# Optimization experiments

Hardware: AMD Instinct MI355X
Metric: run time of the kernel (lower is better)

## Reference

```python
import jax, jax.numpy as jnp
import numpy as np

B, T, D, H = 4, 2048, 1024, 16
HD = D // H


def setup_inputs() -> dict:
    key = jax.random.key(0)
    ks = jax.random.split(key, 10)
    s = 1.0 / np.sqrt(D)
    # xavier_uniform bound for wbias [T,T]: sqrt(6/(T+T))
    wb_bound = float(np.sqrt(6.0 / (T + T)))
    return {
        "x": jax.random.normal(ks[0], (B, T, D), dtype=jnp.float32),
        "Wq": jax.random.normal(ks[1], (D, D), dtype=jnp.float32) * s,
        "bq": jnp.zeros((D,), dtype=jnp.float32),
        "Wk": jax.random.normal(ks[2], (D, D), dtype=jnp.float32) * s,
        "bk": jnp.zeros((D,), dtype=jnp.float32),
        "Wv": jax.random.normal(ks[3], (D, D), dtype=jnp.float32) * s,
        "bv": jnp.zeros((D,), dtype=jnp.float32),
        "Wo": jax.random.normal(ks[4], (D, D), dtype=jnp.float32) * s,
        "bo": jnp.zeros((D,), dtype=jnp.float32),
        "wbias": jax.random.uniform(ks[5], (T, T), dtype=jnp.float32,
                                    minval=-wb_bound, maxval=wb_bound),
    }


def reference(x, Wq, bq, Wk, bk, Wv, bv, Wo, bo, wbias):
    Bc, Tc, Dc = x.shape
    # projections, split heads: [B, H, T, HD]
    def proj(W, b):
        y = x @ W + b
        return y.reshape(Bc, Tc, H, HD).transpose(0, 2, 1, 3)

    Q = proj(Wq, bq)
    K = proj(Wk, bk)
    V = proj(Wv, bv)

    Q_sig = jax.nn.sigmoid(Q)
    eK = jnp.exp(K)                      # [B,H,T,HD]
    ew = jnp.exp(wbias[:Tc, :Tc])        # [T,T]

    num = jnp.einsum('ts,bhsd->bhtd', ew, eK * V)
    den = jnp.einsum('ts,bhsd->bhtd', ew, eK)
    out = Q_sig * (num / den)            # [B,H,T,HD]

    out = out.transpose(0, 2, 1, 3).reshape(Bc, Tc, Dc)
    return out @ Wo + bo
```

## Files before the change

kernel.cpp:

```cpp
#include <hip/hip_runtime.h>
#include <hip/hip_bf16.h>


#define AS1(p) ((const __attribute__((address_space(1))) void*)(p))
#define AS3(p) ((__attribute__((address_space(3))) void*)(p))

typedef _Float16 half8 __attribute__((ext_vector_type(8)));
typedef _Float16 half4v __attribute__((ext_vector_type(4)));
typedef float floatx16 __attribute__((ext_vector_type(16)));
typedef int intx4 __attribute__((ext_vector_type(4)));
typedef int intx8 __attribute__((ext_vector_type(8)));

__device__ __forceinline__ long frag_off(int r, int k) {
  return (long)(((((r >> 5) * 4 + (k >> 4)) * 2 + ((k >> 3) & 1)) * 32 + (r & 31)) * 8 + (k & 7));
}
__device__ __forceinline__ long off8(int r, int k) {
  return (long)((((((r >> 5) * 2 + ((k >> 6) & 1)) * 2 + ((k >> 4) & 1)) * 2 + ((k >> 5) & 1)) * 32 +
                 (r & 31)) * 16 + (k & 15));
}

__global__ __launch_bounds__(256) void prep_all(
    const float* __restrict__ x, const float* __restrict__ wb, const float* __restrict__ Wq,
    const float* __restrict__ Wk, const float* __restrict__ Wv, const float* __restrict__ Wo,
    _Float16* __restrict__ x_h, char* __restrict__ E8, _Float16* __restrict__ WqkvT,
    _Float16* __restrict__ WoT) {
  __shared__ _Float16 lds[64 * 132];
  const int bid = blockIdx.x;
  const int tid = threadIdx.x;

  if (bid < 1024) {
    const int tm = bid >> 4, tk = bid & 15;
    const long tbase = (long)bid * 8192;
#pragma unroll
    for (int p = 0; p < 4; ++p) {
      const int s = p * 256 + tid;
      const int r = ((s >> 8) << 5) + (s & 31);
      const int k = ((s >> 6) & 3) * 16 + ((s >> 5) & 1) * 8;
      const float* sp = x + (long)(tm * 128 + r) * 1024 + tk * 64 + k;
      const float4 v0 = *(const float4*)sp;
      const float4 v1 = *(const float4*)(sp + 4);
      half8 h;
      h[0] = (_Float16)v0.x; h[1] = (_Float16)v0.y; h[2] = (_Float16)v0.z; h[3] = (_Float16)v0.w;
      h[4] = (_Float16)v1.x; h[5] = (_Float16)v1.y; h[6] = (_Float16)v1.z; h[7] = (_Float16)v1.w;
      *(half8*)(x_h + tbase + (long)s * 8) = h;
    }
    return;
  }

  if (bid >= 1536) {
    const int e = bid - 1536;
    const int tt = e >> 4, ts = e & 15;
    char* dst = E8 + (long)e * 16384;
#pragma unroll
    for (int p = 0; p < 16; ++p) {
      const int idx = p * 256 + tid;
      const int r = idx >> 5, k = (idx & 31) * 4;
      const float4 v = *(const float4*)(wb + (long)(tt * 128 + r) * 2048 + ts * 128 + k);
      const float e0 = (__expf(v.x) - 1.0f) * 32.0f, e1 = (__expf(v.y) - 1.0f) * 32.0f;
      const float e2 = (__expf(v.z) - 1.0f) * 32.0f, e3 = (__expf(v.w) - 1.0f) * 32.0f;
      int pk = __builtin_amdgcn_cvt_pk_fp8_f32(e0, e1, 0, false);
      pk = __builtin_amdgcn_cvt_pk_fp8_f32(e2, e3, pk, true);
      *(int*)(dst + off8(r, k)) = pk;
    }
    return;
  }

  const int b2 = bid - 1024;
  const float* src0;
  const float* src1 = nullptr;
  _Float16* dst;
  int tn, tk, cb = 0;
  if (b2 < 128) {
    tn = b2 >> 4; tk = b2 & 15; src0 = Wq; dst = WqkvT;
  } else if (b2 < 384) {
    const int t = b2 - 128;
    tn = 8 + (t >> 4); tk = t & 15; cb = (tn - 8) * 64; src0 = Wk; src1 = Wv; dst = WqkvT;
  } else {
    const int t = b2 - 384;
    tn = t >> 4; tk = t & 15; src0 = Wo; dst = WoT;
  }
  if (!src1) {
#pragma unroll
    for (int p = 0; p < 8; ++p) {
      const int kl = p * 8 + (tid >> 5);
      const int cl = (tid & 31) * 4;
      const float4 v = *(const float4*)(src0 + (long)(tk * 64 + kl) * 1024 + tn * 128 + cl);
      half4v h;
      h[0] = (_Float16)v.x; h[1] = (_Float16)v.y; h[2] = (_Float16)v.z; h[3] = (_Float16)v.w;
      *(half4v*)(lds + kl * 132 + cl) = h;
    }
  } else {
#pragma unroll
    for (int m = 0; m < 2; ++m) {
      const float* s = m ? src1 : src0;
      const int rb = m ? 32 : 0;
#pragma unroll
      for (int p = 0; p < 4; ++p) {
        const int kl = p * 16 + (tid >> 4);
        const int cl = (tid & 15) * 4;
        const int rl = (cl >> 5) * 64 + rb + (cl & 31);
        const float4 v = *(const float4*)(s + (long)(tk * 64 + kl) * 1024 + cb + cl);
        half4v h;
        h[0] = (_Float16)v.x; h[1] = (_Float16)v.y; h[2] = (_Float16)v.z; h[3] = (_Float16)v.w;
        *(half4v*)(lds + kl * 132 + rl) = h;
      }
    }
  }
  __syncthreads();
  const long tbase = (long)(tn * 16 + tk) * 8192;
#pragma unroll
  for (int p = 0; p < 4; ++p) {
    const int s = p * 256 + tid;
    const int r = ((s >> 8) << 5) + (s & 31);
    const int kl = ((s >> 6) & 3) * 16 + ((s >> 5) & 1) * 8;
    half8 h;
#pragma unroll
    for (int j = 0; j < 8; ++j) h[j] = lds[(kl + j) * 132 + r];
    *(half8*)(dst + tbase + (long)s * 8) = h;
  }
}

template <int VM>
__device__ __forceinline__ void aft_phase(int g, const _Float16* __restrict__ Ablk,
                                          const _Float16* __restrict__ Bblk,
                                          _Float16* ring, int tid, int wid, int lane,
                                          int wm, int wn, floatx16 (&acc)[2][2]) {
  const _Float16* slotA = ring + (g & 3) * 4096;
  const _Float16* slotB = ring + 16384 + (g & 3) * 8192;
  half8 af[2][2], bf[2][2];
#pragma unroll
  for (int mt = 0; mt < 2; ++mt)
#pragma unroll
    for (int ks = 0; ks < 2; ++ks)
      af[mt][ks] = *(const half8*)(slotA + ((wm >> 5) + mt) * 1024 + ks * 512 + lane * 8);
#pragma unroll
  for (int nt = 0; nt < 2; ++nt)
#pragma unroll
    for (int ks = 0; ks < 2; ++ks)
      bf[nt][ks] = *(const half8*)(slotB + ((wn >> 5) + nt) * 1024 + ks * 512 + lane * 8);
  const int gs = g + 3;
  if (gs < 32) {
    const int t = gs >> 1;
    const long goff = (long)(tid >> 7) * 2048 + (gs & 1) * 1024 + (tid & 127) * 8;
    _Float16* dA = ring + (gs & 3) * 4096 + wid * 512;
    _Float16* dB = ring + 16384 + (gs & 3) * 8192 + wid * 512;
    __builtin_amdgcn_global_load_lds(AS1(Ablk + (long)t * 8192 + goff), AS3(dA), 16, 0, 0);
    __builtin_amdgcn_global_load_lds(AS1(Bblk + (long)t * 8192 + goff), AS3(dB), 16, 0, 0);
    __builtin_amdgcn_global_load_lds(AS1(Bblk + (long)(16 + t) * 8192 + goff), AS3(dB + 4096),
                                     16, 0, 0);
  }
  asm volatile("s_waitcnt vmcnt(%0)" ::"i"(VM) : "memory");
  __builtin_amdgcn_s_barrier();
  asm volatile("s_waitcnt lgkmcnt(0)" ::: "memory");
  __builtin_amdgcn_s_setprio(1);
#pragma unroll
  for (int ks = 0; ks < 2; ++ks)
#pragma unroll
    for (int mt = 0; mt < 2; ++mt)
#pragma unroll
      for (int nt = 0; nt < 2; ++nt)
        acc[mt][nt] =
            __builtin_amdgcn_mfma_f32_32x32x16_f16(af[mt][ks], bf[nt][ks], acc[mt][nt], 0, 0, 0);
  __builtin_amdgcn_s_setprio(0);
  __builtin_amdgcn_s_barrier();
  asm volatile("" ::: "memory");
}

template <int MODE>
__global__ __launch_bounds__(512, 2) void gemm_bt2(
    const _Float16* __restrict__ A, const _Float16* __restrict__ Bt, void* __restrict__ Cv,
    const float* __restrict__ bias0, const float* __restrict__ bias1,
    const float* __restrict__ bias2, char* __restrict__ Zt8, float* __restrict__ cs) {
  __shared__ __align__(16) _Float16 ring[49152];
  const int tid = threadIdx.x;
  const int wid = tid >> 6, lane = tid & 63;
  const int l32 = lane & 31, khalf = lane >> 5;

  const int f = blockIdx.x;
  const int j = f >> 3;
  const int bxs = (f & 7) * 8 + (j & 7);
  const int bys = j >> 3;
  const int m0 = bxs * 128, n0 = bys * 256;
  const int wm = (wid >> 2) * 64, wn = (wid & 3) * 64;

  const _Float16* Ablk = A + (long)bxs * 131072;
  const _Float16* Bblk = Bt + (long)(bys * 2) * 131072;

#pragma unroll
  for (int g0 = 0; g0 < 3; ++g0) {
    const int t = g0 >> 1;
    const long goff = (long)(tid >> 7) * 2048 + (g0 & 1) * 1024 + (tid & 127) * 8;
    __builtin_amdgcn_global_load_lds(AS1(Ablk + (long)t * 8192 + goff),
                                     AS3(ring + g0 * 4096 + wid * 512), 16, 0, 0);
    __builtin_amdgcn_global_load_lds(AS1(Bblk + (long)t * 8192 + goff),
                                     AS3(ring + 16384 + g0 * 8192 + wid * 512), 16, 0, 0);
    __builtin_amdgcn_global_load_lds(AS1(Bblk + (long)(16 + t) * 8192 + goff),
                                     AS3(ring + 16384 + g0 * 8192 + 4096 + wid * 512), 16, 0, 0);
  }
  asm volatile("s_waitcnt vmcnt(6)" ::: "memory");
  __builtin_amdgcn_s_barrier();
  asm volatile("" ::: "memory");

  floatx16 acc[2][2] = {};
#pragma unroll 1
  for (int gb = 0; gb < 28; gb += 4) {
    aft_phase<6>(gb + 0, Ablk, Bblk, ring, tid, wid, lane, wm, wn, acc);
    aft_phase<6>(gb + 1, Ablk, Bblk, ring, tid, wid, lane, wm, wn, acc);
    aft_phase<6>(gb + 2, Ablk, Bblk, ring, tid, wid, lane, wm, wn, acc);
    aft_phase<6>(gb + 3, Ablk, Bblk, ring, tid, wid, lane, wm, wn, acc);
  }
  aft_phase<6>(28, Ablk, Bblk, ring, tid, wid, lane, wm, wn, acc);
  aft_phase<3>(29, Ablk, Bblk, ring, tid, wid, lane, wm, wn, acc);
  aft_phase<0>(30, Ablk, Bblk, ring, tid, wid, lane, wm, wn, acc);
  aft_phase<0>(31, Ablk, Bblk, ring, tid, wid, lane, wm, wn, acc);

  if (MODE == 0) {
    if (n0 < 1024) {
      _Float16* Qs = (_Float16*)Cv;
#pragma unroll
      for (int mt = 0; mt < 2; ++mt) {
        const long ttile = (m0 + wm + mt * 32) >> 5;
#pragma unroll
        for (int nt = 0; nt < 2; ++nt) {
          const int col = n0 + wn + nt * 32 + l32;
          const float bb = bias0[col];
          const long base = (ttile * 32 + (((n0 + wn) >> 5) + nt)) * 1024;
#pragma unroll
          for (int q = 0; q < 4; ++q) {
            half4v o;
#pragma unroll
            for (int rr = 0; rr < 4; ++rr) {
              const float v = acc[mt][nt][q * 4 + rr] + bb;
              o[rr] = (_Float16)(1.0f / (1.0f + __expf(-v)));
            }
            *(half4v*)(Qs + base + q * 256 + lane * 4) = o;
          }
        }
      }
    } else {
      const int grp = (n0 - 1024 + wn) >> 6;
      const int ch = grp * 32 + l32;
      const float bkc = bias1[ch], bvc = bias2[ch];
      const int jn = grp * 64 + l32;
      const int b = m0 >> 11;
      char* Z8 = Zt8 + (long)b * 4194304 +
                 ((long)(jn >> 7) * 16 + ((m0 & 2047) >> 7)) * 16384;
      const int jnl = jn & 127;
      float sk = 0.f, sz = 0.f;
#pragma unroll
      for (int mt = 0; mt < 2; ++mt) {
#pragma unroll
        for (int q = 0; q < 4; ++q) {
          float ekv[4], ekk[4];
#pragma unroll
          for (int rr = 0; rr < 4; ++rr) {
            const float ek = __expf(acc[mt][0][q * 4 + rr] + bkc);
            const float vv = acc[mt][1][q * 4 + rr] + bvc;
            ekk[rr] = ek;
            ekv[rr] = ek * vv;
            sk += ek;
            sz += ek * vv;
          }
          const int sl = wm + mt * 32 + 4 * khalf + 8 * q;
          int pn = __builtin_amdgcn_cvt_pk_fp8_f32(ekv[0] * 0.25f, ekv[1] * 0.25f, 0, false);
          pn = __builtin_amdgcn_cvt_pk_fp8_f32(ekv[2] * 0.25f, ekv[3] * 0.25f, pn, true);
          int pd = __builtin_amdgcn_cvt_pk_fp8_f32(ekk[0] * 0.25f, ekk[1] * 0.25f, 0, false);
          pd = __builtin_amdgcn_cvt_pk_fp8_f32(ekk[2] * 0.25f, ekk[3] * 0.25f, pd, true);
          *(int*)(Z8 + off8(jnl, sl)) = pn;
          *(int*)(Z8 + off8(jnl + 32, sl)) = pd;
        }
      }
      atomicAdd(&cs[(long)b * 2048 + ch * 2], sz);
      atomicAdd(&cs[(long)b * 2048 + ch * 2 + 1], sk);
    }
    return;
  }

#pragma unroll
  for (int mt = 0; mt < 2; ++mt)
#pragma unroll
    for (int nt = 0; nt < 2; ++nt) {
      const int col = n0 + wn + nt * 32 + l32;
      const float bb = bias0[col];
#pragma unroll
      for (int reg = 0; reg < 16; ++reg) {
        const int row = m0 + wm + mt * 32 + 4 * khalf + 8 * (reg >> 2) + (reg & 3);
        ((float*)Cv)[(long)row * 1024 + col] = acc[mt][nt][reg] + bb;
      }
    }
}

__global__ __launch_bounds__(256) void gemm2_fp8(
    const char* __restrict__ E8, const char* __restrict__ Zt8, _Float16* __restrict__ OH,
    const _Float16* __restrict__ Qsig, const float* __restrict__ cs) {
  __shared__ __align__(16) char sA[16384];
  __shared__ __align__(16) char sB[16384];
  const int tid = threadIdx.x;
  const int wave = tid >> 6, lane = tid & 63;
  const int l32 = lane & 31, khalf = lane >> 5;

  const int f = blockIdx.x + 16 * (blockIdx.y + 16 * blockIdx.z);
  const int nid = (f & 7) * 128 + (f >> 3);
  const int bxs = nid & 15, bys = (nid >> 4) & 15, bzs = nid >> 8;

  const int m0 = bxs * 128, n0 = bys * 128;
  const int wm = (wave >> 1) * 64, wn = (wave & 1) * 64;

  const char* At = E8 + (long)bxs * 16 * 16384;
  const char* Bt = Zt8 + (long)bzs * 4194304 + (long)bys * 16 * 16384;

  floatx16 acc[2][2] = {};

  for (int tk = 0; tk < 16; ++tk) {
    const char* As = At + tk * 16384 + wave * 1024 + lane * 16;
    const char* Bs = Bt + tk * 16384 + wave * 1024 + lane * 16;
#pragma unroll
    for (int c = 0; c < 4; ++c) {
      __builtin_amdgcn_global_load_lds(AS1(As + c * 4096), AS3(sA + c * 4096 + wave * 1024), 16, 0, 0);
      __builtin_amdgcn_global_load_lds(AS1(Bs + c * 4096), AS3(sB + c * 4096 + wave * 1024), 16, 0, 0);
    }
    __syncthreads();
#pragma unroll
    for (int ks = 0; ks < 2; ++ks) {
      intx8 a8[2], b8[2];
#pragma unroll
      for (int i = 0; i < 2; ++i) {
        const char* pa = sA + (((wm >> 5) + i) * 2 + ks) * 2048 + khalf * 512 + l32 * 16;
        const intx4 alo = *(const intx4*)pa;
        const intx4 ahi = *(const intx4*)(pa + 1024);
        a8[i] = __builtin_shufflevector(alo, ahi, 0, 1, 2, 3, 4, 5, 6, 7);
        const char* pb = sB + (((wn >> 5) + i) * 2 + ks) * 2048 + khalf * 512 + l32 * 16;
        const intx4 blo = *(const intx4*)pb;
        const intx4 bhi = *(const intx4*)(pb + 1024);
        b8[i] = __builtin_shufflevector(blo, bhi, 0, 1, 2, 3, 4, 5, 6, 7);
      }
#pragma unroll
      for (int mt = 0; mt < 2; ++mt)
#pragma unroll
        for (int nt = 0; nt < 2; ++nt)
          acc[mt][nt] = __builtin_amdgcn_mfma_scale_f32_32x32x64_f8f6f4(
              a8[mt], b8[nt], acc[mt][nt], 0, 0, 0, 127u, 0, 127u);
    }
    __syncthreads();
  }

  const int ch = ((n0 + wn) >> 6) * 32 + l32;
  const float2 c2 = *(const float2*)(cs + (long)bzs * 2048 + ch * 2);
#pragma unroll
  for (int mt = 0; mt < 2; ++mt) {
    const long ttile = (long)(bzs * 2048 + m0 + wm + mt * 32) >> 5;
    const long qbase = (ttile * 32 + ((n0 + wn) >> 6)) * 1024;
#pragma unroll
    for (int q = 0; q < 4; ++q) {
      const half4v qv = *(const half4v*)(Qsig + qbase + q * 256 + lane * 4);
#pragma unroll
      for (int rr = 0; rr < 4; ++rr) {
        const int reg = q * 4 + rr;
        const float num = c2.x + acc[mt][0][reg] * 0.125f;
        const float den = c2.y + acc[mt][1][reg] * 0.125f;
        const int r = m0 + wm + mt * 32 + 4 * khalf + 8 * q + rr;
        const int R = bzs * 2048 + r;
        const long off = ((long)(R >> 7) * 16 + (ch >> 6)) * 8192 + frag_off(R & 127, ch & 63);
        OH[off] = (_Float16)((float)qv[rr] * num / den);
      }
    }
  }
}

extern "C" void kernel_launch(void* const* d_in, const int* in_sizes, int n_in, void* d_out,
                              int out_size, void* d_ws, size_t ws_size, hipStream_t stream) {
  const float* x = (const float*)d_in[0];
  const float* Wq = (const float*)d_in[1];
  const float* bq = (const float*)d_in[2];
  const float* Wk = (const float*)d_in[3];
  const float* bk = (const float*)d_in[4];
  const float* Wv = (const float*)d_in[5];
  const float* bv = (const float*)d_in[6];
  const float* Wo = (const float*)d_in[7];
  const float* bo = (const float*)d_in[8];
  const float* wb = (const float*)d_in[9];

  char* ws = (char*)d_ws;
  _Float16* x_h = (_Float16*)(ws + 0);
  _Float16* WqkvT = (_Float16*)(ws + 16777216);
  _Float16* WoT = (_Float16*)(ws + 23068672);
  char* E8 = (char*)(ws + 25165824);
  _Float16* Qsig = (_Float16*)(ws + 29360128);
  char* Zt8 = (char*)(ws + 46137344);
  _Float16* OutHead = (_Float16*)(ws + 62914560);
  float* cs = (float*)(ws + 79691776);

  hipMemsetAsync(cs, 0, 4 * 2048 * sizeof(float), stream);

  prep_all<<<1792, 256, 0, stream>>>(x, wb, Wq, Wk, Wv, Wo, x_h, E8, WqkvT, WoT);

  gemm_bt2<0><<<768, 512, 0, stream>>>(x_h, WqkvT, Qsig, bq, bk, bv, Zt8, cs);

  gemm2_fp8<<<dim3(16, 16, 4), 256, 0, stream>>>(E8, Zt8, OutHead, Qsig, cs);

  gemm_bt2<2><<<256, 512, 0, stream>>>(OutHead, WoT, d_out, bo, nullptr, nullptr, nullptr, nullptr);
}
```

Baseline: 250.7 us.

## Use 4-wave GEMM blocks with 64x128 warp tiles and 3-slot LDS ring

The projection GEMMs now run 256-thread blocks in place of 512, so each wave computes a 64x128 output tile (2x4 MFMA accumulators) instead of 64x64. The LDS ring shrinks from four slots to three, and the global-to-LDS prefetch is issued with per-thread precomputed pointers. The vmcnt wait moves after the MFMAs so loads overlap compute. This raises per-wave register reuse and cuts LDS footprint, at the cost of more accumulator registers and fewer waves available to hide latency.

```diff
diff --git a/kernel.cpp b/kernel.cpp
--- a/kernel.cpp
+++ b/kernel.cpp
@@ -120,37 +120,31 @@
   }
 }
 
-template <int VM>
-__device__ __forceinline__ void aft_phase(int g, const _Float16* __restrict__ Ablk,
-                                          const _Float16* __restrict__ Bblk,
-                                          _Float16* ring, int tid, int wid, int lane,
-                                          int wm, int wn, floatx16 (&acc)[2][2]) {
-  const _Float16* slotA = ring + (g & 3) * 4096;
-  const _Float16* slotB = ring + 16384 + (g & 3) * 8192;
-  half8 af[2][2], bf[2][2];
+template <int VM, bool STAGE>
+__device__ __forceinline__ void aft_phase2(
+    const _Float16* rA, const _Float16* rB, _Float16* sAd, _Float16* sBd,
+    const _Float16* gA, const _Float16* gB, int lane, int wm, int wn,
+    floatx16 (&acc)[2][4]) {
+  half8 af[2][2], bf[4][2];
 #pragma unroll
   for (int mt = 0; mt < 2; ++mt)
 #pragma unroll
     for (int ks = 0; ks < 2; ++ks)
-      af[mt][ks] = *(const half8*)(slotA + ((wm >> 5) + mt) * 1024 + ks * 512 + lane * 8);
-#pragma unroll
-  for (int nt = 0; nt < 2; ++nt)
+      af[mt][ks] = *(const half8*)(rA + (((wm >> 5) + mt) * 2 + ks) * 512 + lane * 8);
+#pragma unroll
+  for (int nt = 0; nt < 4; ++nt)
 #pragma unroll
     for (int ks = 0; ks < 2; ++ks)
-      bf[nt][ks] = *(const half8*)(slotB + ((wn >> 5) + nt) * 1024 + ks * 512 + lane * 8);
-  const int gs = g + 3;
-  if (gs < 32) {
-    const int t = gs >> 1;
-    const long goff = (long)(tid >> 7) * 2048 + (gs & 1) * 1024 + (tid & 127) * 8;
-    _Float16* dA = ring + (gs & 3) * 4096 + wid * 512;
-    _Float16* dB = ring + 16384 + (gs & 3) * 8192 + wid * 512;
-    __builtin_amdgcn_global_load_lds(AS1(Ablk + (long)t * 8192 + goff), AS3(dA), 16, 0, 0);
-    __builtin_amdgcn_global_load_lds(AS1(Bblk + (long)t * 8192 + goff), AS3(dB), 16, 0, 0);
-    __builtin_amdgcn_global_load_lds(AS1(Bblk + (long)(16 + t) * 8192 + goff), AS3(dB + 4096),
-                                     16, 0, 0);
-  }
-  asm volatile("s_waitcnt vmcnt(%0)" ::"i"(VM) : "memory");
-  __builtin_amdgcn_s_barrier();
+      bf[nt][ks] = *(const half8*)(rB + (((wn >> 5) + nt) * 2 + ks) * 512 + lane * 8);
+  if (STAGE) {
+#pragma unroll
+    for (int p = 0; p < 2; ++p)
+      __builtin_amdgcn_global_load_lds(AS1(gA + p * 4096), AS3(sAd + p * 2048), 16, 0, 0);
+#pragma unroll
+    for (int q = 0; q < 4; ++q)
+      __builtin_amdgcn_global_load_lds(AS1(gB + (q >> 1) * 131072 + (q & 1) * 4096),
+                                       AS3(sBd + q * 2048), 16, 0, 0);
+  }
   asm volatile("s_waitcnt lgkmcnt(0)" ::: "memory");
   __builtin_amdgcn_s_setprio(1);
 #pragma unroll
@@ -158,20 +152,21 @@
 #pragma unroll
     for (int mt = 0; mt < 2; ++mt)
 #pragma unroll
-      for (int nt = 0; nt < 2; ++nt)
+      for (int nt = 0; nt < 4; ++nt)
         acc[mt][nt] =
             __builtin_amdgcn_mfma_f32_32x32x16_f16(af[mt][ks], bf[nt][ks], acc[mt][nt], 0, 0, 0);
   __builtin_amdgcn_s_setprio(0);
+  asm volatile("s_waitcnt vmcnt(%0)" ::"i"(VM) : "memory");
   __builtin_amdgcn_s_barrier();
   asm volatile("" ::: "memory");
 }
 
 template <int MODE>
-__global__ __launch_bounds__(512, 2) void gemm_bt2(
+__global__ __launch_bounds__(256, 2) void gemm_bt2(
     const _Float16* __restrict__ A, const _Float16* __restrict__ Bt, void* __restrict__ Cv,
     const float* __restrict__ bias0, const float* __restrict__ bias1,
     const float* __restrict__ bias2, char* __restrict__ Zt8, float* __restrict__ cs) {
-  __shared__ __align__(16) _Float16 ring[49152];
+  __shared__ __align__(16) _Float16 ring[36864];
   const int tid = threadIdx.x;
   const int wid = tid >> 6, lane = tid & 63;
   const int l32 = lane & 31, khalf = lane >> 5;
@@ -181,38 +176,48 @@
   const int bxs = (f & 7) * 8 + (j & 7);
   const int bys = j >> 3;
   const int m0 = bxs * 128, n0 = bys * 256;
-  const int wm = (wid >> 2) * 64, wn = (wid & 3) * 64;
-
-  const _Float16* Ablk = A + (long)bxs * 131072;
-  const _Float16* Bblk = Bt + (long)(bys * 2) * 131072;
-
-#pragma unroll
-  for (int g0 = 0; g0 < 3; ++g0) {
-    const int t = g0 >> 1;
-    const long goff = (long)(tid >> 7) * 2048 + (g0 & 1) * 1024 + (tid & 127) * 8;
-    __builtin_amdgcn_global_load_lds(AS1(Ablk + (long)t * 8192 + goff),
-                                     AS3(ring + g0 * 4096 + wid * 512), 16, 0, 0);
-    __builtin_amdgcn_global_load_lds(AS1(Bblk + (long)t * 8192 + goff),
-                                     AS3(ring + 16384 + g0 * 8192 + wid * 512), 16, 0, 0);
-    __builtin_amdgcn_global_load_lds(AS1(Bblk + (long)(16 + t) * 8192 + goff),
-                                     AS3(ring + 16384 + g0 * 8192 + 4096 + wid * 512), 16, 0, 0);
+  const int wm = (wid >> 1) * 64, wn = (wid & 1) * 128;
+
+  const long thrOff = (long)(tid >> 7) * 2048 + (tid & 127) * 8;
+  const _Float16* gA0 = A + (long)bxs * 131072 + thrOff;
+  const _Float16* gB0 = Bt + (long)(bys * 2) * 131072 + thrOff;
+
+  _Float16* ringB = ring + 12288;
+  _Float16* sAt = ring + tid * 8;
+  _Float16* sBt = ringB + tid * 8;
+
+#pragma unroll
+  for (int ph = 0; ph < 2; ++ph) {
+    const _Float16* ga = gA0 + ph * 1024;
+    const _Float16* gb = gB0 + ph * 1024;
+#pragma unroll
+    for (int p = 0; p < 2; ++p)
+      __builtin_amdgcn_global_load_lds(AS1(ga + p * 4096), AS3(sAt + ph * 4096 + p * 2048), 16, 0, 0);
+#pragma unroll
+    for (int q = 0; q < 4; ++q)
+      __builtin_amdgcn_global_load_lds(AS1(gb + (q >> 1) * 131072 + (q & 1) * 4096),
+                                       AS3(sBt + ph * 8192 + q * 2048), 16, 0, 0);
   }
   asm volatile("s_waitcnt vmcnt(6)" ::: "memory");
   __builtin_amdgcn_s_barrier();
   asm volatile("" ::: "memory");
 
-  floatx16 acc[2][2] = {};
-#pragma unroll 1
-  for (int gb = 0; gb < 28; gb += 4) {
-    aft_phase<6>(gb + 0, Ablk, Bblk, ring, tid, wid, lane, wm, wn, acc);
-    aft_phase<6>(gb + 1, Ablk, Bblk, ring, tid, wid, lane, wm, wn, acc);
-    aft_phase<6>(gb + 2, Ablk, Bblk, ring, tid, wid, lane, wm, wn, acc);
-    aft_phase<6>(gb + 3, Ablk, Bblk, ring, tid, wid, lane, wm, wn, acc);
-  }
-  aft_phase<6>(28, Ablk, Bblk, ring, tid, wid, lane, wm, wn, acc);
-  aft_phase<3>(29, Ablk, Bblk, ring, tid, wid, lane, wm, wn, acc);
-  aft_phase<0>(30, Ablk, Bblk, ring, tid, wid, lane, wm, wn, acc);
-  aft_phase<0>(31, Ablk, Bblk, ring, tid, wid, lane, wm, wn, acc);
+  floatx16 acc[2][4] = {};
+
+#pragma unroll
+  for (int pr = 0; pr < 15; ++pr) {
+    const int s0 = (2 * pr) % 3, s1 = (2 * pr + 1) % 3, s2 = (2 * pr + 2) % 3;
+    const _Float16* gA = gA0 + (long)(pr + 1) * 8192;
+    const _Float16* gB = gB0 + (long)(pr + 1) * 8192;
+    aft_phase2<6, true>(ring + s0 * 4096, ringB + s0 * 8192, sAt + s2 * 4096, sBt + s2 * 8192,
+                        gA, gB, lane, wm, wn, acc);
+    aft_phase2<6, true>(ring + s1 * 4096, ringB + s1 * 8192, sAt + s0 * 4096, sBt + s0 * 8192,
+                        gA + 1024, gB + 1024, lane, wm, wn, acc);
+  }
+  aft_phase2<0, false>(ring + 0 * 4096, ringB + 0 * 8192, nullptr, nullptr, nullptr, nullptr,
+                       lane, wm, wn, acc);
+  aft_phase2<0, false>(ring + 1 * 4096, ringB + 1 * 8192, nullptr, nullptr, nullptr, nullptr,
+                       lane, wm, wn, acc);
 
   if (MODE == 0) {
     if (n0 < 1024) {
@@ -221,7 +226,7 @@
       for (int mt = 0; mt < 2; ++mt) {
         const long ttile = (m0 + wm + mt * 32) >> 5;
 #pragma unroll
-        for (int nt = 0; nt < 2; ++nt) {
+        for (int nt = 0; nt < 4; ++nt) {
           const int col = n0 + wn + nt * 32 + l32;
           const float bb = bias0[col];
           const long base = (ttile * 32 + (((n0 + wn) >> 5) + nt)) * 1024;
@@ -238,40 +243,44 @@
         }
       }
     } else {
-      const int grp = (n0 - 1024 + wn) >> 6;
-      const int ch = grp * 32 + l32;
-      const float bkc = bias1[ch], bvc = bias2[ch];
-      const int jn = grp * 64 + l32;
       const int b = m0 >> 11;
-      char* Z8 = Zt8 + (long)b * 4194304 +
-                 ((long)(jn >> 7) * 16 + ((m0 & 2047) >> 7)) * 16384;
-      const int jnl = jn & 127;
-      float sk = 0.f, sz = 0.f;
-#pragma unroll
-      for (int mt = 0; mt < 2; ++mt) {
-#pragma unroll
-        for (int q = 0; q < 4; ++q) {
-          float ekv[4], ekk[4];
-#pragma unroll
-          for (int rr = 0; rr < 4; ++rr) {
-            const float ek = __expf(acc[mt][0][q * 4 + rr] + bkc);
-            const float vv = acc[mt][1][q * 4 + rr] + bvc;
-            ekk[rr] = ek;
-            ekv[rr] = ek * vv;
-            sk += ek;
-            sz += ek * vv;
+      const int g0 = (n0 - 1024 + wn) >> 6;
+#pragma unroll
+      for (int p = 0; p < 2; ++p) {
+        const int grp = g0 + p;
+        const int ch = grp * 32 + l32;
+        const float bkc = bias1[ch], bvc = bias2[ch];
+        const int jn = grp * 64 + l32;
+        char* Z8 = Zt8 + (long)b * 4194304 +
+                   ((long)(jn >> 7) * 16 + ((m0 & 2047) >> 7)) * 16384;
+        const int jnl = jn & 127;
+        float sk = 0.f, sz = 0.f;
+#pragma unroll
+        for (int mt = 0; mt < 2; ++mt) {
+#pragma unroll
+          for (int q = 0; q < 4; ++q) {
+            float ekv[4], ekk[4];
+#pragma unroll
+            for (int rr = 0; rr < 4; ++rr) {
+              const float ek = __expf(acc[mt][2 * p][q * 4 + rr] + bkc);
+              const float vv = acc[mt][2 * p + 1][q * 4 + rr] + bvc;
+              ekk[rr] = ek;
+              ekv[rr] = ek * vv;
+              sk += ek;
+              sz += ek * vv;
+            }
+            const int sl = wm + mt * 32 + 4 * khalf + 8 * q;
+            int pn = __builtin_amdgcn_cvt_pk_fp8_f32(ekv[0] * 0.25f, ekv[1] * 0.25f, 0, false);
+            pn = __builtin_amdgcn_cvt_pk_fp8_f32(ekv[2] * 0.25f, ekv[3] * 0.25f, pn, true);
+            int pd = __builtin_amdgcn_cvt_pk_fp8_f32(ekk[0] * 0.25f, ekk[1] * 0.25f, 0, false);
+            pd = __builtin_amdgcn_cvt_pk_fp8_f32(ekk[2] * 0.25f, ekk[3] * 0.25f, pd, true);
+            *(int*)(Z8 + off8(jnl, sl)) = pn;
+            *(int*)(Z8 + off8(jnl + 32, sl)) = pd;
           }
-          const int sl = wm + mt * 32 + 4 * khalf + 8 * q;
-          int pn = __builtin_amdgcn_cvt_pk_fp8_f32(ekv[0] * 0.25f, ekv[1] * 0.25f, 0, false);
-          pn = __builtin_amdgcn_cvt_pk_fp8_f32(ekv[2] * 0.25f, ekv[3] * 0.25f, pn, true);
-          int pd = __builtin_amdgcn_cvt_pk_fp8_f32(ekk[0] * 0.25f, ekk[1] * 0.25f, 0, false);
-          pd = __builtin_amdgcn_cvt_pk_fp8_f32(ekk[2] * 0.25f, ekk[3] * 0.25f, pd, true);
-          *(int*)(Z8 + off8(jnl, sl)) = pn;
-          *(int*)(Z8 + off8(jnl + 32, sl)) = pd;
         }
-      }
-      atomicAdd(&cs[(long)b * 2048 + ch * 2], sz);
-      atomicAdd(&cs[(long)b * 2048 + ch * 2 + 1], sk);
+        atomicAdd(&cs[(long)b * 2048 + ch * 2], sz);
+        atomicAdd(&cs[(long)b * 2048 + ch * 2 + 1], sk);
+      }
     }
     return;
   }
@@ -279,7 +288,7 @@
 #pragma unroll
   for (int mt = 0; mt < 2; ++mt)
 #pragma unroll
-    for (int nt = 0; nt < 2; ++nt) {
+    for (int nt = 0; nt < 4; ++nt) {
       const int col = n0 + wn + nt * 32 + l32;
       const float bb = bias0[col];
 #pragma unroll
@@ -394,9 +403,9 @@
 
   prep_all<<<1792, 256, 0, stream>>>(x, wb, Wq, Wk, Wv, Wo, x_h, E8, WqkvT, WoT);
 
-  gemm_bt2<0><<<768, 512, 0, stream>>>(x_h, WqkvT, Qsig, bq, bk, bv, Zt8, cs);
+  gemm_bt2<0><<<768, 256, 0, stream>>>(x_h, WqkvT, Qsig, bq, bk, bv, Zt8, cs);
 
   gemm2_fp8<<<dim3(16, 16, 4), 256, 0, stream>>>(E8, Zt8, OutHead, Qsig, cs);
 
-  gemm_bt2<2><<<256, 512, 0, stream>>>(OutHead, WoT, d_out, bo, nullptr, nullptr, nullptr, nullptr);
-}
+  gemm_bt2<2><<<256, 256, 0, stream>>>(OutHead, WoT, d_out, bo, nullptr, nullptr, nullptr, nullptr);
+}
```

After: 251.1 us. Within noise of the previous version (+0.1%).

## Restructure FP8 AFT GEMM into 256x256 tiles with triple-buffered LDS ring

Applied to the files above, without the earlier changes.

The FP8 mixing GEMM goes from 128x128 tiles with 256 threads and a load-sync-compute loop to 256x256 tiles with 512 threads. K-slices are prefetched through a three-slot LDS ring using global_load_lds, with waitcnt/barrier pipelining and raised wave priority around the MFMAs. Each wave now computes 2x4 MFMA tiles, which raises data reuse and cuts global traffic per FLOP. In exchange the grid shrinks from 1024 to 256 blocks at 96KB LDS each, roughly one block per CU, so tail effects and lower occupancy become a risk. The phase-read indexing in the other GEMM is also rewritten into an algebraically identical form.

```diff
diff --git a/kernel.cpp b/kernel.cpp
--- a/kernel.cpp
+++ b/kernel.cpp
@@ -132,12 +132,12 @@
   for (int mt = 0; mt < 2; ++mt)
 #pragma unroll
     for (int ks = 0; ks < 2; ++ks)
-      af[mt][ks] = *(const half8*)(slotA + ((wm >> 5) + mt) * 1024 + ks * 512 + lane * 8);
+      af[mt][ks] = *(const half8*)(slotA + (((wm >> 5) + mt) * 2 + ks) * 512 + lane * 8);
 #pragma unroll
   for (int nt = 0; nt < 2; ++nt)
 #pragma unroll
     for (int ks = 0; ks < 2; ++ks)
-      bf[nt][ks] = *(const half8*)(slotB + ((wn >> 5) + nt) * 1024 + ks * 512 + lane * 8);
+      bf[nt][ks] = *(const half8*)(slotB + (((wn >> 5) + nt) * 2 + ks) * 512 + lane * 8);
   const int gs = g + 3;
   if (gs < 32) {
     const int t = gs >> 1;
@@ -290,78 +290,130 @@
     }
 }
 
-__global__ __launch_bounds__(256) void gemm2_fp8(
+template <int VM, bool STAGE, int SLOT>
+__device__ __forceinline__ void g2_phase(int g, char* __restrict__ ringA, char* __restrict__ ringB,
+                                         const char* At0, const char* At1,
+                                         const char* Bt0, const char* Bt1,
+                                         int tid, int lane, int wm, int wn,
+                                         floatx16 (&acc)[2][4]) {
+  const int l32 = lane & 31, khalf = lane >> 5;
+  intx8 a8[2], b8[4];
+#pragma unroll
+  for (int mt = 0; mt < 2; ++mt) {
+    const int G = (wm >> 5) + mt;
+    const char* pa = ringA + SLOT * 16384 + (G >> 2) * 8192 + (G & 3) * 2048 + khalf * 512 + l32 * 16;
+    const intx4 alo = *(const intx4*)pa;
+    const intx4 ahi = *(const intx4*)(pa + 1024);
+    a8[mt] = __builtin_shufflevector(alo, ahi, 0, 1, 2, 3, 4, 5, 6, 7);
+  }
+#pragma unroll
+  for (int nt = 0; nt < 4; ++nt) {
+    const int Gn = (wn >> 5) + nt;
+    const char* pb = ringB + SLOT * 16384 + (Gn >> 2) * 8192 + (Gn & 3) * 2048 + khalf * 512 + l32 * 16;
+    const intx4 blo = *(const intx4*)pb;
+    const intx4 bhi = *(const intx4*)(pb + 1024);
+    b8[nt] = __builtin_shufflevector(blo, bhi, 0, 1, 2, 3, 4, 5, 6, 7);
+  }
+  if (STAGE) {
+    const int ks = g + 2;
+    constexpr int SS = (SLOT + 2) % 3;
+    const long gsrc = (long)(ks >> 1) * 16384 + (long)(tid >> 7) * 4096 + (long)(ks & 1) * 2048 +
+                      (tid & 127) * 16;
+    char* dA = ringA + SS * 16384 + tid * 16;
+    char* dB = ringB + SS * 16384 + tid * 16;
+    __builtin_amdgcn_global_load_lds(AS1(At0 + gsrc), AS3(dA), 16, 0, 0);
+    __builtin_amdgcn_global_load_lds(AS1(At1 + gsrc), AS3(dA + 8192), 16, 0, 0);
+    __builtin_amdgcn_global_load_lds(AS1(Bt0 + gsrc), AS3(dB), 16, 0, 0);
+    __builtin_amdgcn_global_load_lds(AS1(Bt1 + gsrc), AS3(dB + 8192), 16, 0, 0);
+  }
+  if constexpr (VM >= 0) {
+    asm volatile("s_waitcnt vmcnt(%0)" ::"i"(VM) : "memory");
+    __builtin_amdgcn_s_barrier();
+  }
+  asm volatile("s_waitcnt lgkmcnt(0)" ::: "memory");
+  __builtin_amdgcn_s_setprio(1);
+#pragma unroll
+  for (int mt = 0; mt < 2; ++mt)
+#pragma unroll
+    for (int nt = 0; nt < 4; ++nt)
+      acc[mt][nt] = __builtin_amdgcn_mfma_scale_f32_32x32x64_f8f6f4(
+          a8[mt], b8[nt], acc[mt][nt], 0, 0, 0, 127u, 0, 127u);
+  __builtin_amdgcn_s_setprio(0);
+  if constexpr (VM >= 0) {
+    __builtin_amdgcn_s_barrier();
+    asm volatile("" ::: "memory");
+  }
+}
+
+__global__ __launch_bounds__(512, 1) void gemm2_fp8(
     const char* __restrict__ E8, const char* __restrict__ Zt8, _Float16* __restrict__ OH,
     const _Float16* __restrict__ Qsig, const float* __restrict__ cs) {
-  __shared__ __align__(16) char sA[16384];
-  __shared__ __align__(16) char sB[16384];
+  __shared__ __align__(16) char ring[98304];
+  char* ringA = ring;
+  char* ringB = ring + 49152;
   const int tid = threadIdx.x;
-  const int wave = tid >> 6, lane = tid & 63;
+  const int wid = tid >> 6, lane = tid & 63;
   const int l32 = lane & 31, khalf = lane >> 5;
 
-  const int f = blockIdx.x + 16 * (blockIdx.y + 16 * blockIdx.z);
-  const int nid = (f & 7) * 128 + (f >> 3);
-  const int bxs = nid & 15, bys = (nid >> 4) & 15, bzs = nid >> 8;
-
-  const int m0 = bxs * 128, n0 = bys * 128;
-  const int wm = (wave >> 1) * 64, wn = (wave & 1) * 64;
-
-  const char* At = E8 + (long)bxs * 16 * 16384;
-  const char* Bt = Zt8 + (long)bzs * 4194304 + (long)bys * 16 * 16384;
-
-  floatx16 acc[2][2] = {};
-
-  for (int tk = 0; tk < 16; ++tk) {
-    const char* As = At + tk * 16384 + wave * 1024 + lane * 16;
-    const char* Bs = Bt + tk * 16384 + wave * 1024 + lane * 16;
-#pragma unroll
-    for (int c = 0; c < 4; ++c) {
-      __builtin_amdgcn_global_load_lds(AS1(As + c * 4096), AS3(sA + c * 4096 + wave * 1024), 16, 0, 0);
-      __builtin_amdgcn_global_load_lds(AS1(Bs + c * 4096), AS3(sB + c * 4096 + wave * 1024), 16, 0, 0);
-    }
-    __syncthreads();
-#pragma unroll
-    for (int ks = 0; ks < 2; ++ks) {
-      intx8 a8[2], b8[2];
-#pragma unroll
-      for (int i = 0; i < 2; ++i) {
-        const char* pa = sA + (((wm >> 5) + i) * 2 + ks) * 2048 + khalf * 512 + l32 * 16;
-        const intx4 alo = *(const intx4*)pa;
-        const intx4 ahi = *(const intx4*)(pa + 1024);
-        a8[i] = __builtin_shufflevector(alo, ahi, 0, 1, 2, 3, 4, 5, 6, 7);
-        const char* pb = sB + (((wn >> 5) + i) * 2 + ks) * 2048 + khalf * 512 + l32 * 16;
-        const intx4 blo = *(const intx4*)pb;
-        const intx4 bhi = *(const intx4*)(pb + 1024);
-        b8[i] = __builtin_shufflevector(blo, bhi, 0, 1, 2, 3, 4, 5, 6, 7);
-      }
-#pragma unroll
-      for (int mt = 0; mt < 2; ++mt)
-#pragma unroll
-        for (int nt = 0; nt < 2; ++nt)
-          acc[mt][nt] = __builtin_amdgcn_mfma_scale_f32_32x32x64_f8f6f4(
-              a8[mt], b8[nt], acc[mt][nt], 0, 0, 0, 127u, 0, 127u);
-    }
-    __syncthreads();
-  }
-
-  const int ch = ((n0 + wn) >> 6) * 32 + l32;
-  const float2 c2 = *(const float2*)(cs + (long)bzs * 2048 + ch * 2);
+  const int f = blockIdx.x;
+  const int bxs = f & 7;
+  const int bys = (f >> 3) & 7;
+  const int bzs = f >> 6;
+  const int m0 = bxs * 256;
+  const int wm = (wid >> 1) * 64, wn = (wid & 1) * 128;
+
+  const char* At0 = E8 + (long)(bxs * 2) * 262144;
+  const char* At1 = At0 + 262144;
+  const char* Bt0 = Zt8 + (long)bzs * 4194304 + (long)(bys * 2) * 262144;
+  const char* Bt1 = Bt0 + 262144;
+
+#pragma unroll
+  for (int ks = 0; ks < 2; ++ks) {
+    const long gsrc = (long)(tid >> 7) * 4096 + (long)(ks & 1) * 2048 + (tid & 127) * 16;
+    char* dA = ringA + ks * 16384 + tid * 16;
+    char* dB = ringB + ks * 16384 + tid * 16;
+    __builtin_amdgcn_global_load_lds(AS1(At0 + gsrc), AS3(dA), 16, 0, 0);
+    __builtin_amdgcn_global_load_lds(AS1(At1 + gsrc), AS3(dA + 8192), 16, 0, 0);
+    __builtin_amdgcn_global_load_lds(AS1(Bt0 + gsrc), AS3(dB), 16, 0, 0);
+    __builtin_amdgcn_global_load_lds(AS1(Bt1 + gsrc), AS3(dB + 8192), 16, 0, 0);
+  }
+  asm volatile("s_waitcnt vmcnt(4)" ::: "memory");
+  __builtin_amdgcn_s_barrier();
+  asm volatile("" ::: "memory");
+
+  floatx16 acc[2][4] = {};
+#pragma unroll 1
+  for (int gb = 0; gb < 30; gb += 3) {
+    g2_phase<4, true, 0>(gb + 0, ringA, ringB, At0, At1, Bt0, Bt1, tid, lane, wm, wn, acc);
+    g2_phase<4, true, 1>(gb + 1, ringA, ringB, At0, At1, Bt0, Bt1, tid, lane, wm, wn, acc);
+    g2_phase<4, true, 2>(gb + 2, ringA, ringB, At0, At1, Bt0, Bt1, tid, lane, wm, wn, acc);
+  }
+  g2_phase<0, false, 0>(30, ringA, ringB, At0, At1, Bt0, Bt1, tid, lane, wm, wn, acc);
+  g2_phase<-1, false, 1>(31, ringA, ringB, At0, At1, Bt0, Bt1, tid, lane, wm, wn, acc);
+
+  const int g32b = bys * 4 + (wn >> 6);
 #pragma unroll
   for (int mt = 0; mt < 2; ++mt) {
     const long ttile = (long)(bzs * 2048 + m0 + wm + mt * 32) >> 5;
-    const long qbase = (ttile * 32 + ((n0 + wn) >> 6)) * 1024;
-#pragma unroll
-    for (int q = 0; q < 4; ++q) {
-      const half4v qv = *(const half4v*)(Qsig + qbase + q * 256 + lane * 4);
-#pragma unroll
-      for (int rr = 0; rr < 4; ++rr) {
-        const int reg = q * 4 + rr;
-        const float num = c2.x + acc[mt][0][reg] * 0.125f;
-        const float den = c2.y + acc[mt][1][reg] * 0.125f;
-        const int r = m0 + wm + mt * 32 + 4 * khalf + 8 * q + rr;
-        const int R = bzs * 2048 + r;
-        const long off = ((long)(R >> 7) * 16 + (ch >> 6)) * 8192 + frag_off(R & 127, ch & 63);
-        OH[off] = (_Float16)((float)qv[rr] * num / den);
+#pragma unroll
+    for (int p = 0; p < 2; ++p) {
+      const int g32 = g32b + p;
+      const int ch = g32 * 32 + l32;
+      const float2 c2 = *(const float2*)(cs + (long)bzs * 2048 + ch * 2);
+      const long qbase = (ttile * 32 + g32) * 1024;
+#pragma unroll
+      for (int q = 0; q < 4; ++q) {
+        const half4v qv = *(const half4v*)(Qsig + qbase + q * 256 + lane * 4);
+#pragma unroll
+        for (int rr = 0; rr < 4; ++rr) {
+          const int reg = q * 4 + rr;
+          const float num = c2.x + acc[mt][2 * p][reg] * 0.125f;
+          const float den = c2.y + acc[mt][2 * p + 1][reg] * 0.125f;
+          const int r = m0 + wm + mt * 32 + 4 * khalf + 8 * q + rr;
+          const int R = bzs * 2048 + r;
+          const long off = ((long)(R >> 7) * 16 + (ch >> 6)) * 8192 + frag_off(R & 127, ch & 63);
+          OH[off] = (_Float16)((float)qv[rr] * num / den);
+        }
       }
     }
   }
@@ -396,7 +448,7 @@
 
   gemm_bt2<0><<<768, 512, 0, stream>>>(x_h, WqkvT, Qsig, bq, bk, bv, Zt8, cs);
 
-  gemm2_fp8<<<dim3(16, 16, 4), 256, 0, stream>>>(E8, Zt8, OutHead, Qsig, cs);
+  gemm2_fp8<<<256, 512, 0, stream>>>(E8, Zt8, OutHead, Qsig, cs);
 
   gemm_bt2<2><<<256, 512, 0, stream>>>(OutHead, WoT, d_out, bo, nullptr, nullptr, nullptr, nullptr);
 }
```

After: 246.7 us. Within noise of the previous version (-1.6%).
